# Performance work log

Hardware: AMD Instinct MI355X
Metric: run time of the kernel (lower is better)

Reference implementation:

```python
import jax, jax.numpy as jnp
import numpy as np


def qz(x, width=8, frac=4):
    """Fixed-point fake-quant (MASE integer quantizer) with straight-through estimator."""
    step = 2.0 ** (-frac)
    lo = float(-(2 ** (width - 1)))
    hi = float(2 ** (width - 1) - 1)
    q = jnp.clip(jnp.round(x / step), lo, hi) * step
    return x + jax.lax.stop_gradient(q - x)


def qlinear(x, w, b=None):
    # quantize activations (8,4) and weights (8,7), dequantized GEMM
    y = qz(x, 8, 4) @ qz(w, 8, 7).T
    if b is not None:
        y = y + qz(b, 8, 7)
    return y


def setup_inputs() -> dict:
    key = jax.random.key(0)
    ks = jax.random.split(key, 14)
    B, N, C, HID = 4, 1024, 1024, 4096
    g = lambda k, shape, sc: jax.random.normal(k, shape, jnp.float32) * sc
    return {
        "x": g(ks[0], (B, N, C), 1.0),
        "q_w": g(ks[1], (C, C), 0.05),
        "kv_w": g(ks[2], (2 * C, C), 0.05),
        "proj_w": g(ks[3], (C, C), 0.05),
        "proj_b": jnp.zeros((C,), jnp.float32),
        "fc1_w": g(ks[4], (HID, C), 0.05),
        "fc1_b": jnp.zeros((HID,), jnp.float32),
        "fc2_w": g(ks[5], (C, HID), 0.05),
        "fc2_b": jnp.zeros((C,), jnp.float32),
        "aff1_w": g(ks[6], (1,), 1.0),
        "aff1_b": g(ks[7], (1,), 0.5),
        "aff2_w": g(ks[8], (1,), 1.0),
        "aff2_b": g(ks[9], (1,), 0.5),
    }


def reference(x, q_w, kv_w, proj_w, proj_b, fc1_w, fc1_b, fc2_w, fc2_b,
              aff1_w, aff1_b, aff2_w, aff2_b):
    B, N, C = x.shape
    H = 16
    D = C // H
    scale = D ** (-0.5)

    def affine(t, w, b):
        # quantized mul then quantized add (fixed_affine)
        t = qz(t, 8, 4) * qz(w, 8, 4)
        return qz(t, 8, 4) + qz(b, 8, 4)

    # ---- attention branch ----
    h = affine(x, aff1_w, aff1_b)
    q = qlinear(h, q_w).reshape(B, N, H, D).transpose(0, 2, 1, 3)      # [B,H,N,D]
    kv = qlinear(h, kv_w).reshape(B, N, 2, H, D).transpose(2, 0, 3, 1, 4)
    k, v = kv[0], kv[1]                                                 # [B,H,N,D]
    attn = jnp.einsum('bhnd,bhmd->bhnm', qz(q, 8, 4), qz(k, 8, 4))     # quant matmul
    attn = jax.nn.softmax(qz(attn * scale, 8, 4), axis=-1)             # QHashSoftmax
    attn = qz(attn, 8, 7)
    z = jnp.einsum('bhnm,bhmd->bhnd', qz(attn, 8, 7), qz(v, 8, 4))     # quant matmul
    z = z.transpose(0, 2, 1, 3).reshape(B, N, C)
    z = qlinear(z, proj_w, proj_b)
    x = qz(x, 8, 4) + qz(z, 8, 4)                                      # add1

    # ---- mlp branch ----
    h = affine(x, aff2_w, aff2_b)
    m = qlinear(h, fc1_w, fc1_b)
    m = qz(jax.nn.relu(m), 8, 4)                                       # quant relu
    m = qlinear(m, fc2_w, fc2_b)
    return qz(x, 8, 4) + qz(m, 8, 4)                                   # add2
```

## Files before the change

kernel.cpp:

```cpp
#include <hip/hip_runtime.h>

typedef unsigned short u16;
typedef __attribute__((ext_vector_type(4))) float f32x4;
typedef __attribute__((ext_vector_type(8))) short short8;
typedef __attribute__((ext_vector_type(4))) unsigned short u16x4;
typedef __attribute__((ext_vector_type(8))) unsigned short u16x8;

__device__ __forceinline__ float clampf(float x, float lo, float hi){ return fminf(fmaxf(x, lo), hi); }
__device__ __forceinline__ float qz44i(float x){ return clampf(rintf(x*16.f), -128.f, 127.f); }
__device__ __forceinline__ float qz44v(float x){ return qz44i(x)*0.0625f; }
__device__ __forceinline__ float qz87v(float x){ return clampf(rintf(x*128.f), -128.f, 127.f)*0.0078125f; }
__device__ __forceinline__ u16 bfbits(float f){ return (u16)(__float_as_uint(f) >> 16); }

__device__ __forceinline__ void gll16(const void* g, void* l){
  __builtin_amdgcn_global_load_lds((const __attribute__((address_space(1))) void*)g,
                                   (__attribute__((address_space(3))) void*)l, 16, 0, 0);
}

__global__ __launch_bounds__(256) void kquantw5(const float* __restrict__ w0, u16* __restrict__ o0,
                                                const float* __restrict__ w1, u16* __restrict__ o1,
                                                const float* __restrict__ w2, u16* __restrict__ o2,
                                                const float* __restrict__ w3, u16* __restrict__ o3,
                                                const float* __restrict__ w4, u16* __restrict__ o4){
  int v = blockIdx.x*256 + threadIdx.x;
  const float* w; u16* o; int base;
  if      (v <  262144){ w = w0; o = o0; base = 0;       }
  else if (v <  786432){ w = w1; o = o1; base = 262144;  }
  else if (v < 1048576){ w = w2; o = o2; base = 786432;  }
  else if (v < 2097152){ w = w3; o = o3; base = 1048576; }
  else                 { w = w4; o = o4; base = 2097152; }
  int i = (v - base)*4;
  float4 val = *(const float4*)(w + i);
  u16x4 r;
  r.x = bfbits(qz87v(val.x)); r.y = bfbits(qz87v(val.y));
  r.z = bfbits(qz87v(val.z)); r.w = bfbits(qz87v(val.w));
  *(u16x4*)(o + i) = r;
}

__global__ __launch_bounds__(256) void kaffine(const float* __restrict__ x, const float* __restrict__ aw,
                                               const float* __restrict__ ab, u16* __restrict__ o, int n){
  int i = (blockIdx.x*256 + threadIdx.x)*4;
  if (i >= n) return;
  float awv = qz44v(aw[0]);
  float abi = qz44i(ab[0]);
  float4 v = *(const float4*)(x + i);
  float in[4] = {v.x, v.y, v.z, v.w};
  u16x4 r;
  #pragma unroll
  for (int k=0;k<4;++k){
    float t  = qz44v(in[k]) * awv;
    float hi = clampf(qz44i(t) + abi, -128.f, 127.f);
    ((u16*)&r)[k] = bfbits(hi*0.0625f);
  }
  *(u16x4*)(o + i) = r;
}

__global__ __launch_bounds__(256) void ktransv(const u16* __restrict__ KVb, u16* __restrict__ VT){
  __shared__ u16 t[64][72];
  int nt = blockIdx.x;
  int bh = blockIdx.y;
  int b = bh >> 4, h = bh & 15;
  int tid = threadIdx.x;
  int nl = tid >> 2, d0 = (tid & 3)*16;
  const u16* src = KVb + (size_t)(b*1024 + nt*64 + nl)*2048 + 1024 + h*64 + d0;
  u16x8 v0 = *(const u16x8*)(src);
  u16x8 v1 = *(const u16x8*)(src + 8);
  #pragma unroll
  for (int k=0;k<8;++k) t[nl][d0+k]   = ((u16*)&v0)[k];
  #pragma unroll
  for (int k=0;k<8;++k) t[nl][d0+8+k] = ((u16*)&v1)[k];
  __syncthreads();
  int dl = tid >> 2, n0 = (tid & 3)*16;
  u16x8 o0, o1;
  #pragma unroll
  for (int k=0;k<8;++k) ((u16*)&o0)[k] = t[n0+k][dl];
  #pragma unroll
  for (int k=0;k<8;++k) ((u16*)&o1)[k] = t[n0+8+k][dl];
  u16* dst = VT + (size_t)bh*65536 + (size_t)dl*1024 + nt*64 + n0;
  *(u16x8*)(dst)     = o0;
  *(u16x8*)(dst + 8) = o1;
}

template<int EPI>
__global__ __launch_bounds__(256) void kgemm(
    const u16* __restrict__ A, const u16* __restrict__ Bw,
    const float* __restrict__ bias, const float* __restrict__ extra,
    u16* __restrict__ outB, float* __restrict__ outF,
    int M, int N, int K)
{
  __shared__ char As[128*64*2];
  __shared__ char Bs[128*64*2];
  const int tid = threadIdx.x, lane = tid & 63, w = tid >> 6;
  const int bm = blockIdx.y*128, bn = blockIdx.x*128;
  const int wr = (w>>1)*64, wc = (w&1)*64;
  const int srow = lane>>3;
  const int scol = (((lane&7) ^ srow) & 7)*8;
  const int mrow = lane & 15, kg = lane >> 4, swz = (lane & 7) << 4;

  const u16* Ab = A  + (size_t)bm*K;
  const u16* Bb = Bw + (size_t)bn*K;

  f32x4 acc[4][4];
  #pragma unroll
  for (int i=0;i<4;++i)
    #pragma unroll
    for (int j=0;j<4;++j) acc[i][j] = (f32x4){0.f,0.f,0.f,0.f};

  for (int k0 = 0; k0 < K; k0 += 64){
    #pragma unroll
    for (int c=0;c<4;++c){
      int ch = w*4 + c;
      int row = ch*8 + srow;
      gll16(Ab + (size_t)row*K + k0 + scol, As + ch*1024);
      gll16(Bb + (size_t)row*K + k0 + scol, Bs + ch*1024);
    }
    __syncthreads();
    #pragma unroll
    for (int ks=0; ks<2; ++ks){
      const int cb = (64*ks + 16*kg) ^ swz;
      short8 av[4], bv[4];
      #pragma unroll
      for (int i=0;i<4;++i) av[i] = *(const short8*)(As + (wr + i*16 + mrow)*128 + cb);
      #pragma unroll
      for (int j=0;j<4;++j) bv[j] = *(const short8*)(Bs + (wc + j*16 + mrow)*128 + cb);
      #pragma unroll
      for (int i=0;i<4;++i)
        #pragma unroll
        for (int j=0;j<4;++j)
          acc[i][j] = __builtin_amdgcn_mfma_f32_16x16x32_bf16(av[i], bv[j], acc[i][j], 0, 0, 0);
    }
    __syncthreads();
  }

  #pragma unroll
  for (int i=0;i<4;++i){
    #pragma unroll
    for (int j=0;j<4;++j){
      #pragma unroll
      for (int r=0;r<4;++r){
        int row = bm + wr + i*16 + 4*kg + r;
        int col = bn + wc + j*16 + mrow;
        float y = acc[i][j][r];
        size_t idx = (size_t)row*N + col;
        if (EPI == 0){
          outB[idx] = bfbits(qz44v(y));
        } else if (EPI == 1){
          y += qz87v(bias[col]);
          outF[idx] = qz44v(extra[idx]) + qz44v(y);
        } else if (EPI == 2){
          y += qz87v(bias[col]);
          y = fmaxf(y, 0.f);
          outB[idx] = bfbits(qz44v(y));
        } else {
          y += qz87v(bias[col]);
          outF[idx] = qz44v(extra[idx]) + qz44v(y);
        }
      }
    }
  }
}

template<int EPI>
__global__ __launch_bounds__(256) void kgemm64(
    const u16* __restrict__ A, const u16* __restrict__ Bw,
    const float* __restrict__ bias, const float* __restrict__ extra,
    u16* __restrict__ outB, float* __restrict__ outF,
    int M, int N, int K)
{
  __shared__ char As[128*64*2];
  __shared__ char Bs[64*64*2];
  const int tid = threadIdx.x, lane = tid & 63, w = tid >> 6;
  const int bm = blockIdx.y*128, bn = blockIdx.x*64;
  const int wr = w*32;
  const int srow = lane>>3;
  const int scol = (((lane&7) ^ srow) & 7)*8;
  const int mrow = lane & 15, kg = lane >> 4, swz = (lane & 7) << 4;

  const u16* Ab = A  + (size_t)bm*K;
  const u16* Bb = Bw + (size_t)bn*K;

  f32x4 acc[2][4];
  #pragma unroll
  for (int i=0;i<2;++i)
    #pragma unroll
    for (int j=0;j<4;++j) acc[i][j] = (f32x4){0.f,0.f,0.f,0.f};

  for (int k0 = 0; k0 < K; k0 += 64){
    #pragma unroll
    for (int c=0;c<4;++c){
      int ch = w*4 + c;
      int row = ch*8 + srow;
      gll16(Ab + (size_t)row*K + k0 + scol, As + ch*1024);
    }
    #pragma unroll
    for (int c=0;c<2;++c){
      int ch = w*2 + c;
      int row = ch*8 + srow;
      gll16(Bb + (size_t)row*K + k0 + scol, Bs + ch*1024);
    }
    __syncthreads();
    #pragma unroll
    for (int ks=0; ks<2; ++ks){
      const int cb = (64*ks + 16*kg) ^ swz;
      short8 av[2], bv[4];
      #pragma unroll
      for (int i=0;i<2;++i) av[i] = *(const short8*)(As + (wr + i*16 + mrow)*128 + cb);
      #pragma unroll
      for (int j=0;j<4;++j) bv[j] = *(const short8*)(Bs + (j*16 + mrow)*128 + cb);
      #pragma unroll
      for (int i=0;i<2;++i)
        #pragma unroll
        for (int j=0;j<4;++j)
          acc[i][j] = __builtin_amdgcn_mfma_f32_16x16x32_bf16(av[i], bv[j], acc[i][j], 0, 0, 0);
    }
    __syncthreads();
  }

  #pragma unroll
  for (int i=0;i<2;++i){
    #pragma unroll
    for (int j=0;j<4;++j){
      #pragma unroll
      for (int r=0;r<4;++r){
        int row = bm + wr + i*16 + 4*kg + r;
        int col = bn + j*16 + mrow;
        float y = acc[i][j][r];
        size_t idx = (size_t)row*N + col;
        if (EPI == 0){
          outB[idx] = bfbits(qz44v(y));
        } else if (EPI == 1){
          y += qz87v(bias[col]);
          outF[idx] = qz44v(extra[idx]) + qz44v(y);
        } else if (EPI == 2){
          y += qz87v(bias[col]);
          y = fmaxf(y, 0.f);
          outB[idx] = bfbits(qz44v(y));
        } else {
          y += qz87v(bias[col]);
          outF[idx] = qz44v(extra[idx]) + qz44v(y);
        }
      }
    }
  }
}

__device__ __forceinline__ void compute_s(const char* Qs, const char* Ks,
                                          int w, int mrow, int kg, int swz, f32x4 (&s)[2][8]){
  short8 a[2][2];
  #pragma unroll
  for (int i=0;i<2;++i)
    #pragma unroll
    for (int ks=0;ks<2;++ks)
      a[i][ks] = *(const short8*)(Qs + (w*32 + i*16 + mrow)*128 + ((64*ks + 16*kg) ^ swz));
  #pragma unroll
  for (int i=0;i<2;++i)
    #pragma unroll
    for (int jf=0;jf<8;++jf) s[i][jf] = (f32x4){0.f,0.f,0.f,0.f};
  #pragma unroll
  for (int jf=0;jf<8;++jf){
    short8 b0 = *(const short8*)(Ks + (jf*16 + mrow)*128 + ((16*kg) ^ swz));
    short8 b1 = *(const short8*)(Ks + (jf*16 + mrow)*128 + ((64 + 16*kg) ^ swz));
    #pragma unroll
    for (int i=0;i<2;++i){
      s[i][jf] = __builtin_amdgcn_mfma_f32_16x16x32_bf16(a[i][0], b0, s[i][jf], 0, 0, 0);
      s[i][jf] = __builtin_amdgcn_mfma_f32_16x16x32_bf16(a[i][1], b1, s[i][jf], 0, 0, 0);
    }
  }
}

__global__ __launch_bounds__(256) void kattn(const u16* __restrict__ Qb, const u16* __restrict__ KVb,
                                             const u16* __restrict__ VT, u16* __restrict__ zq)
{
  __shared__ char Qs[128*128];
  __shared__ char Ks[128*128];
  __shared__ char Ps[128*256];
  __shared__ char Vs[64*128];
  __shared__ float exp_t[256];
  const int tid = threadIdx.x, lane = tid & 63, w = tid >> 6;
  const int qt = blockIdx.x, bh = blockIdx.y;
  const int b = bh >> 4, h = bh & 15;
  const int srow = lane >> 3;
  const int scol = (((lane&7) ^ srow) & 7)*8;
  const int mrow = lane & 15, kg = lane >> 4, swz = (lane & 7) << 4;
  const size_t q0 = (size_t)(b*1024 + qt*128);
  const u16* Vg = VT + (size_t)bh*65536;

  exp_t[tid & 255] = expf(-(float)(tid & 255) * 0.0625f);

  #pragma unroll
  for (int c=0;c<4;++c){
    int ch = w*4 + c; int r = ch*8 + srow;
    gll16(Qb + (q0 + r)*1024 + h*64 + scol, Qs + ch*1024);
  }

  float m[2][4], Z[2][4];
  #pragma unroll
  for (int i=0;i<2;++i)
    #pragma unroll
    for (int r=0;r<4;++r){ m[i][r] = -128.f; Z[i][r] = 0.f; }

  for (int kt=0; kt<8; ++kt){
    #pragma unroll
    for (int c=0;c<4;++c){
      int ch = w*4 + c; int r = ch*8 + srow;
      gll16(KVb + (size_t)(b*1024 + kt*128 + r)*2048 + h*64 + scol, Ks + ch*1024);
    }
    __syncthreads();
    f32x4 s[2][8];
    compute_s(Qs, Ks, w, mrow, kg, swz, s);
    #pragma unroll
    for (int i=0;i<2;++i){
      #pragma unroll
      for (int r=0;r<4;++r){
        float li[8];
        float tm = -128.f;
        #pragma unroll
        for (int jf=0;jf<8;++jf){
          li[jf] = clampf(rintf(s[i][jf][r]*2.f), -128.f, 127.f);
          tm = fmaxf(tm, li[jf]);
        }
        #pragma unroll
        for (int off=1; off<16; off<<=1) tm = fmaxf(tm, __shfl_xor(tm, off));
        float ts = 0.f;
        #pragma unroll
        for (int jf=0;jf<8;++jf) ts += exp_t[(int)(tm - li[jf])];
        #pragma unroll
        for (int off=1; off<16; off<<=1) ts += __shfl_xor(ts, off);
        float mo = m[i][r];
        float mn = fmaxf(mo, tm);
        Z[i][r] = Z[i][r]*exp_t[(int)(mn - mo)] + ts*exp_t[(int)(mn - tm)];
        m[i][r] = mn;
      }
    }
    __syncthreads();
  }

  f32x4 zacc[2][4];
  #pragma unroll
  for (int i=0;i<2;++i)
    #pragma unroll
    for (int d=0;d<4;++d) zacc[i][d] = (f32x4){0.f,0.f,0.f,0.f};

  for (int kt=0; kt<8; ++kt){
    #pragma unroll
    for (int c=0;c<4;++c){
      int ch = w*4 + c; int r = ch*8 + srow;
      gll16(KVb + (size_t)(b*1024 + kt*128 + r)*2048 + h*64 + scol, Ks + ch*1024);
    }
    #pragma unroll
    for (int j=0;j<2;++j){
      int cc = j*256 + tid;
      int row = cc >> 3, s16 = cc & 7;
      int col16 = s16 ^ (row & 7);
      gll16(Vg + (size_t)row*1024 + kt*128 + col16*8, Vs + cc*16);
    }
    __syncthreads();
    f32x4 s[2][8];
    compute_s(Qs, Ks, w, mrow, kg, swz, s);
    #pragma unroll
    for (int i=0;i<2;++i){
      #pragma unroll
      for (int r=0;r<4;++r){
        float Mi = m[i][r], zz = Z[i][r];
        int prow = w*32 + i*16 + 4*kg + r;
        int sw2 = (prow & 7) << 4;
        #pragma unroll
        for (int jf=0;jf<8;++jf){
          float li = clampf(rintf(s[i][jf][r]*2.f), -128.f, 127.f);
          float e = exp_t[(int)(Mi - li)];
          float p = e / zz;
          float pi = fminf(rintf(p*128.f), 127.f);
          *(u16*)(Ps + prow*256 + (((jf*16 + mrow)*2) ^ sw2)) = bfbits(pi*0.0078125f);
        }
      }
    }
    #pragma unroll
    for (int msh=0; msh<2; ++msh){
      const int ms = msh;
      const int cbp = (64*ms + 16*kg) ^ swz;
      short8 pa0 = *(const short8*)(Ps + (w*32 +  0 + mrow)*256 + cbp);
      short8 pa1 = *(const short8*)(Ps + (w*32 + 16 + mrow)*256 + cbp);
      #pragma unroll
      for (int df=0; df<4; ++df){
        int vrow = df*16 + mrow;
        short8 vb = *(const short8*)(Vs + vrow*128 + (((msh*4 + kg) ^ (vrow & 7)) << 4));
        zacc[0][df] = __builtin_amdgcn_mfma_f32_16x16x32_bf16(pa0, vb, zacc[0][df], 0, 0, 0);
        zacc[1][df] = __builtin_amdgcn_mfma_f32_16x16x32_bf16(pa1, vb, zacc[1][df], 0, 0, 0);
      }
    }
    __syncthreads();
    #pragma unroll
    for (int j=0;j<2;++j){
      int cc = j*256 + tid;
      int row = cc >> 3, s16 = cc & 7;
      int col16 = s16 ^ (row & 7);
      gll16(Vg + (size_t)row*1024 + kt*128 + 64 + col16*8, Vs + cc*16);
    }
    __syncthreads();
    #pragma unroll
    for (int msh=0; msh<2; ++msh){
      const int ms = 2 + msh;
      const int cbp = (64*ms + 16*kg) ^ swz;
      short8 pa0 = *(const short8*)(Ps + (w*32 +  0 + mrow)*256 + cbp);
      short8 pa1 = *(const short8*)(Ps + (w*32 + 16 + mrow)*256 + cbp);
      #pragma unroll
      for (int df=0; df<4; ++df){
        int vrow = df*16 + mrow;
        short8 vb = *(const short8*)(Vs + vrow*128 + (((msh*4 + kg) ^ (vrow & 7)) << 4));
        zacc[0][df] = __builtin_amdgcn_mfma_f32_16x16x32_bf16(pa0, vb, zacc[0][df], 0, 0, 0);
        zacc[1][df] = __builtin_amdgcn_mfma_f32_16x16x32_bf16(pa1, vb, zacc[1][df], 0, 0, 0);
      }
    }
    __syncthreads();
  }

  #pragma unroll
  for (int i=0;i<2;++i){
    #pragma unroll
    for (int df=0; df<4; ++df){
      #pragma unroll
      for (int r=0;r<4;++r){
        int row = qt*128 + w*32 + i*16 + 4*kg + r;
        int col = df*16 + mrow;
        zq[((size_t)b*1024 + row)*1024 + h*64 + col] = bfbits(qz44v(zacc[i][df][r]));
      }
    }
  }
}

extern "C" void kernel_launch(void* const* d_in, const int* in_sizes, int n_in,
                              void* d_out, int out_size, void* d_ws, size_t ws_size,
                              hipStream_t stream) {
  const float* x      = (const float*)d_in[0];
  const float* q_w    = (const float*)d_in[1];
  const float* kv_w   = (const float*)d_in[2];
  const float* proj_w = (const float*)d_in[3];
  const float* proj_b = (const float*)d_in[4];
  const float* fc1_w  = (const float*)d_in[5];
  const float* fc1_b  = (const float*)d_in[6];
  const float* fc2_w  = (const float*)d_in[7];
  const float* fc2_b  = (const float*)d_in[8];
  const float* aff1_w = (const float*)d_in[9];
  const float* aff1_b = (const float*)d_in[10];
  const float* aff2_w = (const float*)d_in[11];
  const float* aff2_b = (const float*)d_in[12];

  char* ws = (char*)d_ws;
  const size_t MB = 1u << 20;
  u16*   wq_q  = (u16*)(ws + 0*MB);
  u16*   wq_kv = (u16*)(ws + 2*MB);
  u16*   wq_pj = (u16*)(ws + 6*MB);
  u16*   wq_f1 = (u16*)(ws + 8*MB);
  u16*   wq_f2 = (u16*)(ws + 16*MB);
  float* x1    = (float*)(ws + 24*MB);
  u16*   h1q   = (u16*)(ws + 40*MB);
  u16*   Qbuf  = (u16*)(ws + 48*MB);
  u16*   KVb   = (u16*)(ws + 56*MB);
  u16*   VT    = (u16*)(ws + 72*MB);
  u16*   mq    = (u16*)(ws + 56*MB);
  u16*   zq    = h1q;
  u16*   h2q   = Qbuf;

  kquantw5<<<12288, 256, 0, stream>>>(q_w, wq_q, kv_w, wq_kv, proj_w, wq_pj,
                                      fc1_w, wq_f1, fc2_w, wq_f2);

  kaffine<<<4096, 256, 0, stream>>>(x, aff1_w, aff1_b, h1q, 4096*1024);
  kgemm64<0><<<dim3(16,32), 256, 0, stream>>>(h1q, wq_q,  nullptr, nullptr, Qbuf, nullptr, 4096, 1024, 1024);
  kgemm<0><<<dim3(16,32),  256, 0, stream>>>(h1q, wq_kv, nullptr, nullptr, KVb,  nullptr, 4096, 2048, 1024);
  ktransv<<<dim3(16,64), 256, 0, stream>>>(KVb, VT);
  kattn<<<dim3(8,64), 256, 0, stream>>>(Qbuf, KVb, VT, zq);
  kgemm64<1><<<dim3(16,32), 256, 0, stream>>>(zq, wq_pj, proj_b, x, nullptr, x1, 4096, 1024, 1024);

  kaffine<<<4096, 256, 0, stream>>>(x1, aff2_w, aff2_b, h2q, 4096*1024);
  kgemm<2><<<dim3(32,32), 256, 0, stream>>>(h2q, wq_f1, fc1_b, nullptr, mq, nullptr, 4096, 4096, 1024);
  kgemm64<3><<<dim3(16,32), 256, 0, stream>>>(mq, wq_f2, fc2_b, x1, nullptr, (float*)d_out, 4096, 1024, 4096);
}
```

Before: 418.3 us.

## Double-buffer K tiles, keep Q in registers, prefetch V in attention kernel

The attention kernel now loads the Q fragments into registers once and reuses the freed LDS as a second K buffer. The next K tile is prefetched while the current one is used for QK^T, and the first V half of the next tile is issued at the end of the previous iteration, so global loads overlap with compute and fewer barriers are needed. The per-element divide by Z is replaced with a multiply by a precomputed 128/Z. This can change rounding slightly near ties, and the persistent Q registers plus the launch-bounds hint may add register pressure.

```diff
diff --git a/kernel.cpp b/kernel.cpp
--- a/kernel.cpp
+++ b/kernel.cpp
@@ -244,14 +244,8 @@
   }
 }
 
-__device__ __forceinline__ void compute_s(const char* Qs, const char* Ks,
-                                          int w, int mrow, int kg, int swz, f32x4 (&s)[2][8]){
-  short8 a[2][2];
-  #pragma unroll
-  for (int i=0;i<2;++i)
-    #pragma unroll
-    for (int ks=0;ks<2;++ks)
-      a[i][ks] = *(const short8*)(Qs + (w*32 + i*16 + mrow)*128 + ((64*ks + 16*kg) ^ swz));
+__device__ __forceinline__ void compute_s_reg(const short8 (&qa)[2][2], const char* Ks,
+                                              int mrow, int kg, int swz, f32x4 (&s)[2][8]){
   #pragma unroll
   for (int i=0;i<2;++i)
     #pragma unroll
@@ -262,17 +256,17 @@
     short8 b1 = *(const short8*)(Ks + (jf*16 + mrow)*128 + ((64 + 16*kg) ^ swz));
     #pragma unroll
     for (int i=0;i<2;++i){
-      s[i][jf] = __builtin_amdgcn_mfma_f32_16x16x32_bf16(a[i][0], b0, s[i][jf], 0, 0, 0);
-      s[i][jf] = __builtin_amdgcn_mfma_f32_16x16x32_bf16(a[i][1], b1, s[i][jf], 0, 0, 0);
-    }
-  }
-}
-
-__global__ __launch_bounds__(256) void kattn(const u16* __restrict__ Qb, const u16* __restrict__ KVb,
-                                             const u16* __restrict__ VT, u16* __restrict__ zq)
+      s[i][jf] = __builtin_amdgcn_mfma_f32_16x16x32_bf16(qa[i][0], b0, s[i][jf], 0, 0, 0);
+      s[i][jf] = __builtin_amdgcn_mfma_f32_16x16x32_bf16(qa[i][1], b1, s[i][jf], 0, 0, 0);
+    }
+  }
+}
+
+__global__ __launch_bounds__(256, 4) void kattn(const u16* __restrict__ Qb, const u16* __restrict__ KVb,
+                                                const u16* __restrict__ VT, u16* __restrict__ zq)
 {
-  __shared__ char Qs[128*128];
-  __shared__ char Ks[128*128];
+  __shared__ char KsA[128*128];
+  __shared__ char KsB[128*128];
   __shared__ char Ps[128*256];
   __shared__ char Vs[64*128];
   __shared__ float exp_t[256];
@@ -284,14 +278,23 @@
   const int mrow = lane & 15, kg = lane >> 4, swz = (lane & 7) << 4;
   const size_t q0 = (size_t)(b*1024 + qt*128);
   const u16* Vg = VT + (size_t)bh*65536;
+  const u16* Kg = KVb + (size_t)(b*1024)*2048 + h*64;
 
   exp_t[tid & 255] = expf(-(float)(tid & 255) * 0.0625f);
 
   #pragma unroll
   for (int c=0;c<4;++c){
     int ch = w*4 + c; int r = ch*8 + srow;
-    gll16(Qb + (q0 + r)*1024 + h*64 + scol, Qs + ch*1024);
-  }
+    gll16(Qb + (q0 + r)*1024 + h*64 + scol, KsB + ch*1024);
+  }
+  __syncthreads();
+  short8 qa[2][2];
+  #pragma unroll
+  for (int i=0;i<2;++i)
+    #pragma unroll
+    for (int ks=0;ks<2;++ks)
+      qa[i][ks] = *(const short8*)(KsB + (w*32 + i*16 + mrow)*128 + ((64*ks + 16*kg) ^ swz));
+  __syncthreads();
 
   float m[2][4], Z[2][4];
   #pragma unroll
@@ -299,15 +302,25 @@
     #pragma unroll
     for (int r=0;r<4;++r){ m[i][r] = -128.f; Z[i][r] = 0.f; }
 
+  #pragma unroll
+  for (int c=0;c<4;++c){
+    int ch = w*4 + c; int r = ch*8 + srow;
+    gll16(Kg + (size_t)r*2048 + scol, KsA + ch*1024);
+  }
+
   for (int kt=0; kt<8; ++kt){
-    #pragma unroll
-    for (int c=0;c<4;++c){
-      int ch = w*4 + c; int r = ch*8 + srow;
-      gll16(KVb + (size_t)(b*1024 + kt*128 + r)*2048 + h*64 + scol, Ks + ch*1024);
-    }
-    __syncthreads();
+    char* cur = (kt&1) ? KsB : KsA;
+    char* nxt = (kt&1) ? KsA : KsB;
+    __syncthreads();
+    if (kt < 7){
+      #pragma unroll
+      for (int c=0;c<4;++c){
+        int ch = w*4 + c; int r = ch*8 + srow;
+        gll16(Kg + (size_t)((kt+1)*128 + r)*2048 + scol, nxt + ch*1024);
+      }
+    }
     f32x4 s[2][8];
-    compute_s(Qs, Ks, w, mrow, kg, swz, s);
+    compute_s_reg(qa, cur, mrow, kg, swz, s);
     #pragma unroll
     for (int i=0;i<2;++i){
       #pragma unroll
@@ -332,7 +345,6 @@
         m[i][r] = mn;
       }
     }
-    __syncthreads();
   }
 
   f32x4 zacc[2][4];
@@ -341,43 +353,52 @@
     #pragma unroll
     for (int d=0;d<4;++d) zacc[i][d] = (f32x4){0.f,0.f,0.f,0.f};
 
+  #pragma unroll
+  for (int c=0;c<4;++c){
+    int ch = w*4 + c; int r = ch*8 + srow;
+    gll16(Kg + (size_t)r*2048 + scol, KsA + ch*1024);
+  }
+  #pragma unroll
+  for (int j=0;j<2;++j){
+    int cc = j*256 + tid;
+    int row = cc >> 3, s16 = cc & 7;
+    int col16 = s16 ^ (row & 7);
+    gll16(Vg + (size_t)row*1024 + col16*8, Vs + cc*16);
+  }
+
   for (int kt=0; kt<8; ++kt){
-    #pragma unroll
-    for (int c=0;c<4;++c){
-      int ch = w*4 + c; int r = ch*8 + srow;
-      gll16(KVb + (size_t)(b*1024 + kt*128 + r)*2048 + h*64 + scol, Ks + ch*1024);
-    }
-    #pragma unroll
-    for (int j=0;j<2;++j){
-      int cc = j*256 + tid;
-      int row = cc >> 3, s16 = cc & 7;
-      int col16 = s16 ^ (row & 7);
-      gll16(Vg + (size_t)row*1024 + kt*128 + col16*8, Vs + cc*16);
-    }
-    __syncthreads();
+    char* cur = (kt&1) ? KsB : KsA;
+    char* nxt = (kt&1) ? KsA : KsB;
+    __syncthreads();
+    if (kt < 7){
+      #pragma unroll
+      for (int c=0;c<4;++c){
+        int ch = w*4 + c; int r = ch*8 + srow;
+        gll16(Kg + (size_t)((kt+1)*128 + r)*2048 + scol, nxt + ch*1024);
+      }
+    }
     f32x4 s[2][8];
-    compute_s(Qs, Ks, w, mrow, kg, swz, s);
+    compute_s_reg(qa, cur, mrow, kg, swz, s);
     #pragma unroll
     for (int i=0;i<2;++i){
       #pragma unroll
       for (int r=0;r<4;++r){
-        float Mi = m[i][r], zz = Z[i][r];
+        float Mi = m[i][r];
+        float srw = 128.f / Z[i][r];
         int prow = w*32 + i*16 + 4*kg + r;
         int sw2 = (prow & 7) << 4;
         #pragma unroll
         for (int jf=0;jf<8;++jf){
           float li = clampf(rintf(s[i][jf][r]*2.f), -128.f, 127.f);
           float e = exp_t[(int)(Mi - li)];
-          float p = e / zz;
-          float pi = fminf(rintf(p*128.f), 127.f);
+          float pi = fminf(rintf(e*srw), 127.f);
           *(u16*)(Ps + prow*256 + (((jf*16 + mrow)*2) ^ sw2)) = bfbits(pi*0.0078125f);
         }
       }
     }
     #pragma unroll
     for (int msh=0; msh<2; ++msh){
-      const int ms = msh;
-      const int cbp = (64*ms + 16*kg) ^ swz;
+      const int cbp = (64*msh + 16*kg) ^ swz;
       short8 pa0 = *(const short8*)(Ps + (w*32 +  0 + mrow)*256 + cbp);
       short8 pa1 = *(const short8*)(Ps + (w*32 + 16 + mrow)*256 + cbp);
       #pragma unroll
@@ -399,8 +420,7 @@
     __syncthreads();
     #pragma unroll
     for (int msh=0; msh<2; ++msh){
-      const int ms = 2 + msh;
-      const int cbp = (64*ms + 16*kg) ^ swz;
+      const int cbp = (64*(2+msh) + 16*kg) ^ swz;
       short8 pa0 = *(const short8*)(Ps + (w*32 +  0 + mrow)*256 + cbp);
       short8 pa1 = *(const short8*)(Ps + (w*32 + 16 + mrow)*256 + cbp);
       #pragma unroll
@@ -411,7 +431,16 @@
         zacc[1][df] = __builtin_amdgcn_mfma_f32_16x16x32_bf16(pa1, vb, zacc[1][df], 0, 0, 0);
       }
     }
-    __syncthreads();
+    if (kt < 7){
+      __syncthreads();
+      #pragma unroll
+      for (int j=0;j<2;++j){
+        int cc = j*256 + tid;
+        int row = cc >> 3, s16 = cc & 7;
+        int col16 = s16 ^ (row & 7);
+        gll16(Vg + (size_t)row*1024 + (kt+1)*128 + col16*8, Vs + cc*16);
+      }
+    }
   }
 
   #pragma unroll
```

Result: faster. 382.6 us (-8.5%).
